# Kernel tuning notes

Hardware: AMD Instinct MI355X
Metric: run time of the kernel (lower is better)

## Reference

```python
import jax, jax.numpy as jnp
import numpy as np

B, T, V, E, H = 512, 40, 50000, 300, 512


def setup_inputs() -> dict:
    key = jax.random.key(0)
    ks = jax.random.split(key, 8)
    ref_expr_inds = jax.random.randint(ks[0], (B, T), 0, V)
    emb = jax.random.normal(ks[1], (V, E), dtype=jnp.float32) * 0.1
    w = lambda k, s: jax.random.normal(k, s, dtype=jnp.float32) * 0.05
    return dict(
        ref_expr_inds=ref_expr_inds,
        emb=emb,
        w_ih_f=w(ks[2], (3 * H, E)), w_hh_f=w(ks[3], (3 * H, H)),
        b_ih_f=jnp.zeros((3 * H,), jnp.float32), b_hh_f=jnp.zeros((3 * H,), jnp.float32),
        w_ih_b=w(ks[4], (3 * H, E)), w_hh_b=w(ks[5], (3 * H, H)),
        b_ih_b=jnp.zeros((3 * H,), jnp.float32), b_hh_b=jnp.zeros((3 * H,), jnp.float32),
    )


def _gru_dir(x, w_ih, w_hh, b_ih, b_hh):
    """Single-direction GRU (PyTorch math, gate order r,z,n). x: [B,T,E] -> [B,T,H]."""
    gi = jnp.einsum('bte,ge->btg', x, w_ih) + b_ih  # [B,T,3H], precomputed input gates

    def step(h, gi_t):
        gh = h @ w_hh.T + b_hh  # [B,3H]
        ir, iz, inn = jnp.split(gi_t, 3, axis=-1)
        hr, hz, hn = jnp.split(gh, 3, axis=-1)
        r = jax.nn.sigmoid(ir + hr)
        z = jax.nn.sigmoid(iz + hz)
        n = jnp.tanh(inn + r * hn)
        h_new = (1.0 - z) * n + z * h
        return h_new, h_new

    h0 = jnp.zeros((x.shape[0], w_hh.shape[1]), x.dtype)
    _, ys = jax.lax.scan(step, h0, jnp.swapaxes(gi, 0, 1))  # ys: [T,B,H]
    return jnp.swapaxes(ys, 0, 1)


def reference(ref_expr_inds, emb, w_ih_f, w_hh_f, b_ih_f, b_hh_f,
              w_ih_b, w_hh_b, b_ih_b, b_hh_b):
    valid = ref_expr_inds != 0  # True = real token (torch uses y_mask = (inds==0), then pools over ~y_mask)
    x = emb[ref_expr_inds]  # [B,T,E] embedding lookup
    y_f = _gru_dir(x, w_ih_f, w_hh_f, b_ih_f, b_hh_f)
    y_b = _gru_dir(x[:, ::-1], w_ih_b, w_hh_b, b_ih_b, b_hh_b)[:, ::-1]
    y_word = jnp.concatenate([y_f, y_b], axis=-1)  # [B,T,2H]
    neg = jnp.finfo(y_word.dtype).min
    # masked max-pool over valid tokens, vectorized (replaces python per-sample loop)
    y = jnp.max(jnp.where(valid[:, :, None], y_word, neg), axis=1, keepdims=True)  # [B,1,2H]
    return y
```

## Files before the change

kernel.cpp:

```cpp
#include <hip/hip_runtime.h>

typedef unsigned short u16;
typedef unsigned int u32;
typedef unsigned long long u64;
typedef short s16x8 __attribute__((ext_vector_type(8)));
typedef float f32x4 __attribute__((ext_vector_type(4)));
typedef u32 u32x4 __attribute__((ext_vector_type(4)));

#define T_SEQ 40
#define EMB 300
#define KPAD 320
#define NCOL 3072

__device__ __forceinline__ u16 f2bf(float x) {
  u32 u = __builtin_bit_cast(u32, x);
  u32 r = (u + 0x7fffu + ((u >> 16) & 1u)) >> 16;
  return (u16)r;
}
__device__ __forceinline__ float bf2f(u16 h) {
  return __builtin_bit_cast(float, ((u32)h) << 16);
}
#define LOG2E 1.4426950408889634f
__device__ __forceinline__ float sigm(float x) {
  return 1.0f / (1.0f + __builtin_amdgcn_exp2f(-x * LOG2E));
}
__device__ __forceinline__ float fast_tanh(float x) {
  return 1.0f - 2.0f / (1.0f + __builtin_amdgcn_exp2f(2.0f * LOG2E * x));
}

__global__ void k_init(const int* __restrict__ idxs, u64* __restrict__ mask,
                       int* __restrict__ bar) {
  int i = blockIdx.x * 256 + threadIdx.x;
  if (i < 264) __hip_atomic_store(&bar[i], 0, __ATOMIC_RELAXED, __HIP_MEMORY_SCOPE_AGENT);
  if (i < 512) {
    u64 b = 0;
    for (int t = 0; t < T_SEQ; ++t)
      if (idxs[i * T_SEQ + t] != 0) b |= (1ull << t);
    mask[i] = b;
  }
}

__global__ void k_prep_emb(const float* __restrict__ emb, u16* __restrict__ emb16) {
  for (int idx = blockIdx.x * 256 + threadIdx.x; idx < 50000 * 160; idx += 4096 * 256) {
    int row = idx / 160, c2 = idx - row * 160;
    int c0 = 2 * c2;
    float v0 = (c0 < EMB) ? emb[(size_t)row * EMB + c0] : 0.0f;
    float v1 = (c0 + 1 < EMB) ? emb[(size_t)row * EMB + c0 + 1] : 0.0f;
    ((u32*)emb16)[(size_t)row * 160 + c2] = (u32)f2bf(v0) | ((u32)f2bf(v1) << 16);
  }
}

__global__ void k_prep_wih(const float* __restrict__ wf, const float* __restrict__ wb,
                           u16* __restrict__ wih) {
  int n = blockIdx.x, e = threadIdx.x;
  int dir = (n >= 1536);
  int g = n - dir * 1536;
  const float* src = dir ? wb : wf;
  float v = (e < EMB) ? src[(size_t)g * EMB + e] : 0.0f;
  wih[(size_t)n * KPAD + e] = f2bf(v);
}

__global__ void k_prep_whh(const float* __restrict__ wf, const float* __restrict__ wb,
                           u16* __restrict__ w16) {
  int n = blockIdx.x, k = threadIdx.x;
  int dir = (n >= 1536);
  int g = n - dir * 1536;
  float v = (dir ? wb : wf)[(size_t)g * 512 + k];
  w16[(size_t)n * 512 + k] = f2bf(v);
}

__global__ void k_prep_bias(const float* __restrict__ bihf, const float* __restrict__ bihb,
                            const float* __restrict__ bhhf, const float* __restrict__ bhhb,
                            float* __restrict__ bias_ih, float* __restrict__ bias_hh) {
  int i = blockIdx.x * 1024 + threadIdx.x;
  if (i >= 3072) return;
  int dir = (i >= 1536);
  int g = i - dir * 1536;
  bias_ih[i] = dir ? bihb[g] : bihf[g];
  bias_hh[i] = dir ? bhhb[g] : bhhf[g];
}

__global__ __launch_bounds__(256) void k_gi_gemm(
    const int* __restrict__ idxs, const float* __restrict__ emb,
    const u16* __restrict__ emb16, int use_emb16,
    const u16* __restrict__ wih, const float* __restrict__ bias_ih,
    u16* __restrict__ gi) {
  __shared__ __align__(16) char smem[34816];
  u16(*As)[40] = (u16(*)[40])smem;
  u16(*Bs)[40] = (u16(*)[40])(smem + 10240);
  u16(*Cs)[136] = (u16(*)[136])smem;

  const int m0 = blockIdx.x * 128;
  const int n0 = blockIdx.y * 128;
  const int t = threadIdx.x;
  const int w = t >> 6, l = t & 63;
  const int wm = (w >> 1) * 64, wn = (w & 1) * 64;
  const int lr = l & 15, lg = l >> 4;

  f32x4 acc[4][4];
#pragma unroll
  for (int i = 0; i < 4; ++i)
#pragma unroll
    for (int j = 0; j < 4; ++j) acc[i][j] = (f32x4)0.0f;

  const int arow = t >> 1, aseg = t & 1;
  const int tok = idxs[m0 + arow];
  const float* aerow = emb + (size_t)tok * EMB;
  const u16* aerow16 = emb16 + (size_t)tok * KPAD;
  const u16* brow_p = wih + (size_t)(n0 + arow) * KPAD;

  for (int kc = 0; kc < 10; ++kc) {
    const int k0 = kc * 32;
    if (use_emb16) {
      *(uint4*)&As[arow][aseg * 16] = *(const uint4*)(aerow16 + k0 + aseg * 16);
      *(uint4*)(&As[arow][aseg * 16] + 8) = *(const uint4*)(aerow16 + k0 + aseg * 16 + 8);
    } else {
      int cb = k0 + aseg * 16;
      u16* d = &As[arow][aseg * 16];
      if (cb + 15 < EMB) {
        const float4* s = (const float4*)(aerow + cb);
        float4 v0 = s[0], v1 = s[1], v2 = s[2], v3 = s[3];
        uint4 w0, w1;
        w0.x = (u32)f2bf(v0.x) | ((u32)f2bf(v0.y) << 16);
        w0.y = (u32)f2bf(v0.z) | ((u32)f2bf(v0.w) << 16);
        w0.z = (u32)f2bf(v1.x) | ((u32)f2bf(v1.y) << 16);
        w0.w = (u32)f2bf(v1.z) | ((u32)f2bf(v1.w) << 16);
        w1.x = (u32)f2bf(v2.x) | ((u32)f2bf(v2.y) << 16);
        w1.y = (u32)f2bf(v2.z) | ((u32)f2bf(v2.w) << 16);
        w1.z = (u32)f2bf(v3.x) | ((u32)f2bf(v3.y) << 16);
        w1.w = (u32)f2bf(v3.z) | ((u32)f2bf(v3.w) << 16);
        *(uint4*)d = w0;
        *(uint4*)(d + 8) = w1;
      } else {
#pragma unroll
        for (int e = 0; e < 16; ++e) {
          int c = cb + e;
          d[e] = (c < EMB) ? f2bf(aerow[c]) : (u16)0;
        }
      }
    }
    {
      const u16* s = brow_p + k0 + aseg * 16;
      u16* d = &Bs[arow][aseg * 16];
      *(uint4*)d = *(const uint4*)s;
      *(uint4*)(d + 8) = *(const uint4*)(s + 8);
    }
    __syncthreads();
    s16x8 av[4], bv[4];
#pragma unroll
    for (int i = 0; i < 4; ++i) av[i] = *(const s16x8*)&As[wm + i * 16 + lr][lg * 8];
#pragma unroll
    for (int j = 0; j < 4; ++j) bv[j] = *(const s16x8*)&Bs[wn + j * 16 + lr][lg * 8];
#pragma unroll
    for (int i = 0; i < 4; ++i)
#pragma unroll
      for (int j = 0; j < 4; ++j)
        acc[i][j] = __builtin_amdgcn_mfma_f32_16x16x32_bf16(av[i], bv[j], acc[i][j], 0, 0, 0);
    __syncthreads();
  }

  float bj[4];
#pragma unroll
  for (int j = 0; j < 4; ++j) bj[j] = bias_ih[n0 + wn + j * 16 + lr];
#pragma unroll
  for (int i = 0; i < 4; ++i)
#pragma unroll
    for (int j = 0; j < 4; ++j)
#pragma unroll
      for (int r = 0; r < 4; ++r)
        Cs[wm + i * 16 + lg * 4 + r][wn + j * 16 + lr] = f2bf(acc[i][j][r] + bj[j]);
  __syncthreads();
#pragma unroll
  for (int rr = t >> 4; rr < 128; rr += 16) {
    const int cseg = (t & 15) * 8;
    __builtin_nontemporal_store(*(const u32x4*)&Cs[rr][cseg],
                                (u32x4*)(gi + (size_t)(m0 + rr) * NCOL + n0 + cseg));
  }
}

__global__ __launch_bounds__(512) void k_gru_persist(
    const u16* __restrict__ whh16, const float* __restrict__ bias_hh,
    const u16* __restrict__ gi, const u64* __restrict__ mask, u32* __restrict__ hpk,
    float* __restrict__ ymax, int* __restrict__ bar) {
  extern __shared__ u16 wlds[];
  __shared__ int s_claim[2];
  __shared__ int s_arrive;
  const int t = threadIdx.x;
  if (t == 0) {
    int xcd;
    asm volatile("s_getreg_b32 %0, hwreg(HW_REG_XCC_ID)" : "=s"(xcd));
    xcd &= 7;
    int slot =
        __hip_atomic_fetch_add(&bar[256 + xcd], 1, __ATOMIC_RELAXED, __HIP_MEMORY_SCOPE_AGENT);
    s_claim[0] = xcd;
    s_claim[1] = slot & 31;
    s_arrive = 0;
  }
  __syncthreads();
  const int mt = s_claim[0];
  const int slot = s_claim[1];
  const int dir = slot & 1;
  const int jt = slot >> 1;
  const int m0 = mt * 64, j0 = jt * 32;
  const int wbase = dir * 1536;
  const int w = t >> 6, l = t & 63, lr = l & 15, lg = l >> 4;
  const int mh = w >> 1, jh = w & 1;

  for (int c = t; c < 6144; c += 512) {
    const int col = c % 96, kcg = c / 96;
    const int g = col >> 5, jj = col & 31;
    const int k = (kcg >> 2) * 32 + (kcg & 3) * 8;
    const size_t off = (size_t)(wbase + g * 512 + j0 + jj) * 512 + k;
    *(uint4*)&wlds[c * 8] = *(const uint4*)(whh16 + off);
  }
  const int jg = j0 + jh * 16 + lr;
  const float bR = bias_hh[wbase + jg];
  const float bZ = bias_hh[wbase + 512 + jg];
  const float bN = bias_hh[wbase + 1024 + jg];
  u64 mk[4];
  float hprev[4], ym[4];
  int mrow[4];
#pragma unroll
  for (int r = 0; r < 4; ++r) {
    mrow[r] = m0 + mh * 16 + lg * 4 + r;
    mk[r] = mask[mrow[r]];
    hprev[r] = 0.0f;
    ym[r] = -3.402823466e38f;
  }
  __syncthreads();

  const int pollidx = mt * 32 + 2 * (l & 15) + dir;
  const size_t aoff = (size_t)(mh * 16 + lr) * 512;

  for (int s = 0; s < T_SEQ; ++s) {
    const int tok = dir ? (T_SEQ - 1 - s) : s;

    if (s > 0) {
      const u32 tgt = (u32)s;
      while (true) {
        u32 f = __hip_atomic_load((u32*)&bar[pollidx], __ATOMIC_RELAXED,
                                  __HIP_MEMORY_SCOPE_AGENT);
        if (__all(f >= tgt)) break;
        __builtin_amdgcn_s_sleep(1);
      }
    }

    u16 gr[4], gz[4], gn[4];
#pragma unroll
    for (int r = 0; r < 4; ++r) {
      const size_t gb = ((size_t)mrow[r] * T_SEQ + tok) * NCOL + wbase + jg;
      gr[r] = __builtin_nontemporal_load(gi + gb);
      gz[r] = __builtin_nontemporal_load(gi + gb + 512);
      gn[r] = __builtin_nontemporal_load(gi + gb + 1024);
    }

    f32x4 acc[3];
    acc[0] = acc[1] = acc[2] = (f32x4)0.0f;
    if (s > 0) {
      const u32* hs = hpk + ((((size_t)(s & 7)) * 2 + dir) * 8 + mt) * 32768;
#pragma unroll
      for (int kc = 0; kc < 16; ++kc) {
        const uint4* ap = (const uint4*)(hs + aoff + kc * 32 + lg * 8);
        uint4 q0 = ap[0], q1 = ap[1];
        u32 hw[8];
        *(uint4*)&hw[0] = q0;
        *(uint4*)&hw[4] = q1;
        u32 ahw[4], alw[4];
#pragma unroll
        for (int i = 0; i < 4; ++i) {
          ahw[i] = (hw[2 * i] & 0xFFFFu) | (hw[2 * i + 1] << 16);
          alw[i] = (hw[2 * i] >> 16) | (hw[2 * i + 1] & 0xFFFF0000u);
        }
        const s16x8 ah = __builtin_bit_cast(s16x8, *(uint4*)ahw);
        const s16x8 al = __builtin_bit_cast(s16x8, *(uint4*)alw);
        const int bb = ((kc * 4 + lg) * 96 + jh * 16 + lr) * 8;
#pragma unroll
        for (int g = 0; g < 3; ++g) {
          const s16x8 bh = *(const s16x8*)&wlds[bb + g * 256];
          acc[g] = __builtin_amdgcn_mfma_f32_16x16x32_bf16(ah, bh, acc[g], 0, 0, 0);
          acc[g] = __builtin_amdgcn_mfma_f32_16x16x32_bf16(al, bh, acc[g], 0, 0, 0);
        }
      }
    }

    u32 hpack[4];
#pragma unroll
    for (int r = 0; r < 4; ++r) {
      const float rg = sigm(bf2f(gr[r]) + acc[0][r] + bR);
      const float zg = sigm(bf2f(gz[r]) + acc[1][r] + bZ);
      const float ng = fast_tanh(bf2f(gn[r]) + rg * (acc[2][r] + bN));
      const float hn = (1.0f - zg) * ng + zg * hprev[r];
      hprev[r] = hn;
      const u16 hh = f2bf(hn);
      const u16 hl = f2bf(hn - bf2f(hh));
      hpack[r] = (u32)hh | ((u32)hl << 16);
      if ((mk[r] >> tok) & 1ull) ym[r] = fmaxf(ym[r], hn);
    }

    if (s < T_SEQ - 1) {
      u32* hd = hpk + ((((size_t)((s + 1) & 7)) * 2 + dir) * 8 + mt) * 32768;
#pragma unroll
      for (int r = 0; r < 4; ++r)
        hd[(size_t)(mh * 16 + lg * 4 + r) * 512 + jg] = hpack[r];
      asm volatile("s_waitcnt vmcnt(0)" ::: "memory");
      if (l == 0) {
        int old = atomicAdd(&s_arrive, 1);
        if (old == 8 * (s + 1) - 1)
          __hip_atomic_store((u32*)&bar[mt * 32 + slot], (u32)(s + 1), __ATOMIC_RELAXED,
                             __HIP_MEMORY_SCOPE_AGENT);
      }
    }
  }

#pragma unroll
  for (int r = 0; r < 4; ++r)
    ymax[(size_t)mrow[r] * 1024 + dir * 512 + jg] = ym[r];
}

extern "C" void kernel_launch(void* const* d_in, const int* in_sizes, int n_in,
                              void* d_out, int out_size, void* d_ws, size_t ws_size,
                              hipStream_t stream) {
  const int* idxs = (const int*)d_in[0];
  const float* emb = (const float*)d_in[1];
  const float* wihf = (const float*)d_in[2];
  const float* whhf = (const float*)d_in[3];
  const float* bihf = (const float*)d_in[4];
  const float* bhhf = (const float*)d_in[5];
  const float* wihb = (const float*)d_in[6];
  const float* whhb = (const float*)d_in[7];
  const float* bihb = (const float*)d_in[8];
  const float* bhhb = (const float*)d_in[9];
  float* ymax = (float*)d_out;

  char* ws = (char*)d_ws;
  u16* whh16 = (u16*)(ws + 0);
  u16* wih = (u16*)(ws + 6291456);
  float* bias_ih = (float*)(ws + 8257536);
  float* bias_hh = (float*)(ws + 8269824);
  u64* mask = (u64*)(ws + 8282112);
  int* bar = (int*)(ws + 8286208);
  u16* emb16 = (u16*)(ws + 8290304);
  u32* hpk = (u32*)(ws + 8290304);
  u16* gi = (u16*)(ws + 40290304);
  const int use_emb16 = (ws_size >= 166119424ull) ? 1 : 0;

  k_init<<<2, 256, 0, stream>>>(idxs, mask, bar);
  if (use_emb16) k_prep_emb<<<4096, 256, 0, stream>>>(emb, emb16);
  k_prep_wih<<<3072, 320, 0, stream>>>(wihf, wihb, wih);
  k_prep_whh<<<3072, 512, 0, stream>>>(whhf, whhb, whh16);
  k_prep_bias<<<3, 1024, 0, stream>>>(bihf, bihb, bhhf, bhhb, bias_ih, bias_hh);
  k_gi_gemm<<<dim3(160, 24), 256, 0, stream>>>(idxs, emb, emb16, use_emb16, wih, bias_ih, gi);

  hipFuncSetAttribute((const void*)k_gru_persist,
                      hipFuncAttributeMaxDynamicSharedMemorySize, 98304);
  k_gru_persist<<<dim3(256), dim3(512), 98304, stream>>>(whh16, bias_hh, gi, mask, hpk,
                                                         ymax, bar);
}
```

Before: 797.9 us.

## Remap persistent GRU work so each XCD owns one direction with 16-slot sync groups

Each XCD now handles one direction and a 128-row batch tile, and each block covers 32 hidden columns across all 8 waves. Previously an XCD held 64 rows for both directions in 32-block groups. Barrier groups shrink from 32 to 16 blocks, and blocks whose slot is 16 or above exit immediately. Other changes: the gate-input loads move ahead of the spin-wait so they overlap it, the s_sleep backoff becomes a busy FMA loop, and h-state loads are software-prefetched one k-chunk ahead. The aim is lower cross-block synchronization latency per timestep, at the cost of more MFMA work per wave and more idle launched blocks.

Measured after the change: 1.178 ms. 1.48x slower.

```diff
diff --git a/kernel.cpp b/kernel.cpp
--- a/kernel.cpp
+++ b/kernel.cpp
@@ -31,7 +31,7 @@
 __global__ void k_init(const int* __restrict__ idxs, u64* __restrict__ mask,
                        int* __restrict__ bar) {
   int i = blockIdx.x * 256 + threadIdx.x;
-  if (i < 264) __hip_atomic_store(&bar[i], 0, __ATOMIC_RELAXED, __HIP_MEMORY_SCOPE_AGENT);
+  if (i < 272) __hip_atomic_store(&bar[i], 0, __ATOMIC_RELAXED, __HIP_MEMORY_SCOPE_AGENT);
   if (i < 512) {
     u64 b = 0;
     for (int t = 0; t < T_SEQ; ++t)
@@ -193,18 +193,19 @@
     int slot =
         __hip_atomic_fetch_add(&bar[256 + xcd], 1, __ATOMIC_RELAXED, __HIP_MEMORY_SCOPE_AGENT);
     s_claim[0] = xcd;
-    s_claim[1] = slot & 31;
+    s_claim[1] = slot;
     s_arrive = 0;
   }
   __syncthreads();
-  const int mt = s_claim[0];
+  const int xcd = s_claim[0];
   const int slot = s_claim[1];
-  const int dir = slot & 1;
-  const int jt = slot >> 1;
-  const int m0 = mt * 64, j0 = jt * 32;
+  if (slot >= 16) return;
+
+  const int mt = xcd >> 1, dir = xcd & 1, jt = slot;
+  const int m0 = mt * 128, j0 = jt * 32;
   const int wbase = dir * 1536;
   const int w = t >> 6, l = t & 63, lr = l & 15, lg = l >> 4;
-  const int mh = w >> 1, jh = w & 1;
+  u32* flags = (u32*)bar + xcd * 16;
 
   for (int c = t; c < 6144; c += 512) {
     const int col = c % 96, kcg = c / 96;
@@ -213,58 +214,82 @@
     const size_t off = (size_t)(wbase + g * 512 + j0 + jj) * 512 + k;
     *(uint4*)&wlds[c * 8] = *(const uint4*)(whh16 + off);
   }
-  const int jg = j0 + jh * 16 + lr;
-  const float bR = bias_hh[wbase + jg];
-  const float bZ = bias_hh[wbase + 512 + jg];
-  const float bN = bias_hh[wbase + 1024 + jg];
+
+  int jg[2];
+  jg[0] = j0 + lr;
+  jg[1] = j0 + 16 + lr;
+  float bR[2], bZ[2], bN[2];
+#pragma unroll
+  for (int jn = 0; jn < 2; ++jn) {
+    bR[jn] = bias_hh[wbase + jg[jn]];
+    bZ[jn] = bias_hh[wbase + 512 + jg[jn]];
+    bN[jn] = bias_hh[wbase + 1024 + jg[jn]];
+  }
   u64 mk[4];
-  float hprev[4], ym[4];
   int mrow[4];
+  float hprev[2][4], ym[2][4];
 #pragma unroll
   for (int r = 0; r < 4; ++r) {
-    mrow[r] = m0 + mh * 16 + lg * 4 + r;
+    mrow[r] = m0 + w * 16 + lg * 4 + r;
     mk[r] = mask[mrow[r]];
-    hprev[r] = 0.0f;
-    ym[r] = -3.402823466e38f;
+#pragma unroll
+    for (int jn = 0; jn < 2; ++jn) {
+      hprev[jn][r] = 0.0f;
+      ym[jn][r] = -3.402823466e38f;
+    }
   }
   __syncthreads();
 
-  const int pollidx = mt * 32 + 2 * (l & 15) + dir;
-  const size_t aoff = (size_t)(mh * 16 + lr) * 512;
+  const size_t arow = (size_t)(w * 16 + lr) * 512 + lg * 8;
+  const u32* fp = &flags[l & 15];
 
   for (int s = 0; s < T_SEQ; ++s) {
     const int tok = dir ? (T_SEQ - 1 - s) : s;
 
+    u16 gr[2][4], gz[2][4], gn[2][4];
+#pragma unroll
+    for (int jn = 0; jn < 2; ++jn)
+#pragma unroll
+      for (int r = 0; r < 4; ++r) {
+        const size_t gb = ((size_t)mrow[r] * T_SEQ + tok) * NCOL + wbase + jg[jn];
+        gr[jn][r] = __builtin_nontemporal_load(gi + gb);
+        gz[jn][r] = __builtin_nontemporal_load(gi + gb + 512);
+        gn[jn][r] = __builtin_nontemporal_load(gi + gb + 1024);
+      }
+
+    f32x4 acc[3][2];
+#pragma unroll
+    for (int g = 0; g < 3; ++g) acc[g][0] = acc[g][1] = (f32x4)0.0f;
+
     if (s > 0) {
-      const u32 tgt = (u32)s;
-      while (true) {
-        u32 f = __hip_atomic_load((u32*)&bar[pollidx], __ATOMIC_RELAXED,
-                                  __HIP_MEMORY_SCOPE_AGENT);
-        if (__all(f >= tgt)) break;
-        __builtin_amdgcn_s_sleep(1);
-      }
-    }
-
-    u16 gr[4], gz[4], gn[4];
-#pragma unroll
-    for (int r = 0; r < 4; ++r) {
-      const size_t gb = ((size_t)mrow[r] * T_SEQ + tok) * NCOL + wbase + jg;
-      gr[r] = __builtin_nontemporal_load(gi + gb);
-      gz[r] = __builtin_nontemporal_load(gi + gb + 512);
-      gn[r] = __builtin_nontemporal_load(gi + gb + 1024);
-    }
-
-    f32x4 acc[3];
-    acc[0] = acc[1] = acc[2] = (f32x4)0.0f;
-    if (s > 0) {
-      const u32* hs = hpk + ((((size_t)(s & 7)) * 2 + dir) * 8 + mt) * 32768;
+      {
+        const u32 tgt = (u32)s;
+        float ba = 1.0000001f;
+        const float bm = 1.0000002f;
+        while (true) {
+          u32 f = __hip_atomic_load(fp, __ATOMIC_RELAXED, __HIP_MEMORY_SCOPE_AGENT);
+          if (__all(f >= tgt)) break;
+#pragma unroll
+          for (int b = 0; b < 24; ++b)
+            asm volatile("v_fmac_f32 %0, %1, %1" : "+v"(ba) : "v"(bm));
+        }
+        asm volatile("" ::"v"(ba));
+      }
+
+      const u32* hs = hpk + ((size_t)((s & 7) * 2 + dir) * 4 + mt) * 65536;
+      const u32* ap = hs + arow;
+      uint4 c0 = *(const uint4*)(ap);
+      uint4 c1 = *(const uint4*)(ap + 4);
 #pragma unroll
       for (int kc = 0; kc < 16; ++kc) {
-        const uint4* ap = (const uint4*)(hs + aoff + kc * 32 + lg * 8);
-        uint4 q0 = ap[0], q1 = ap[1];
+        uint4 n0 = c0, n1 = c1;
+        if (kc < 15) {
+          n0 = *(const uint4*)(ap + (kc + 1) * 32);
+          n1 = *(const uint4*)(ap + (kc + 1) * 32 + 4);
+        }
         u32 hw[8];
-        *(uint4*)&hw[0] = q0;
-        *(uint4*)&hw[4] = q1;
+        *(uint4*)&hw[0] = c0;
+        *(uint4*)&hw[4] = c1;
         u32 ahw[4], alw[4];
 #pragma unroll
         for (int i = 0; i < 4; ++i) {
@@ -273,48 +298,65 @@
         }
         const s16x8 ah = __builtin_bit_cast(s16x8, *(uint4*)ahw);
         const s16x8 al = __builtin_bit_cast(s16x8, *(uint4*)alw);
-        const int bb = ((kc * 4 + lg) * 96 + jh * 16 + lr) * 8;
-#pragma unroll
-        for (int g = 0; g < 3; ++g) {
-          const s16x8 bh = *(const s16x8*)&wlds[bb + g * 256];
-          acc[g] = __builtin_amdgcn_mfma_f32_16x16x32_bf16(ah, bh, acc[g], 0, 0, 0);
-          acc[g] = __builtin_amdgcn_mfma_f32_16x16x32_bf16(al, bh, acc[g], 0, 0, 0);
+        const int bb = (kc * 4 + lg) * 96;
+#pragma unroll
+        for (int g = 0; g < 3; ++g)
+#pragma unroll
+          for (int jn = 0; jn < 2; ++jn) {
+            const s16x8 bh = *(const s16x8*)&wlds[(bb + g * 32 + jn * 16 + lr) * 8];
+            acc[g][jn] = __builtin_amdgcn_mfma_f32_16x16x32_bf16(ah, bh, acc[g][jn], 0, 0, 0);
+            acc[g][jn] = __builtin_amdgcn_mfma_f32_16x16x32_bf16(al, bh, acc[g][jn], 0, 0, 0);
+          }
+        c0 = n0;
+        c1 = n1;
+      }
+    }
+
+    float hn_v[2][4];
+#pragma unroll
+    for (int jn = 0; jn < 2; ++jn)
+#pragma unroll
+      for (int r = 0; r < 4; ++r) {
+        const float rg = sigm(bf2f(gr[jn][r]) + acc[0][jn][r] + bR[jn]);
+        const float zg = sigm(bf2f(gz[jn][r]) + acc[1][jn][r] + bZ[jn]);
+        const float ng = fast_tanh(bf2f(gn[jn][r]) + rg * (acc[2][jn][r] + bN[jn]));
+        hn_v[jn][r] = (1.0f - zg) * ng + zg * hprev[jn][r];
+      }
+
+    if (s < T_SEQ - 1) {
+      u32* hd = hpk + ((size_t)(((s + 1) & 7) * 2 + dir) * 4 + mt) * 65536;
+#pragma unroll
+      for (int jn = 0; jn < 2; ++jn)
+#pragma unroll
+        for (int r = 0; r < 4; ++r) {
+          const float hn = hn_v[jn][r];
+          const u16 hh = f2bf(hn);
+          const u16 hl = f2bf(hn - bf2f(hh));
+          hd[(size_t)(w * 16 + lg * 4 + r) * 512 + jg[jn]] = (u32)hh | ((u32)hl << 16);
         }
-      }
-    }
-
-    u32 hpack[4];
-#pragma unroll
-    for (int r = 0; r < 4; ++r) {
-      const float rg = sigm(bf2f(gr[r]) + acc[0][r] + bR);
-      const float zg = sigm(bf2f(gz[r]) + acc[1][r] + bZ);
-      const float ng = fast_tanh(bf2f(gn[r]) + rg * (acc[2][r] + bN));
-      const float hn = (1.0f - zg) * ng + zg * hprev[r];
-      hprev[r] = hn;
-      const u16 hh = f2bf(hn);
-      const u16 hl = f2bf(hn - bf2f(hh));
-      hpack[r] = (u32)hh | ((u32)hl << 16);
-      if ((mk[r] >> tok) & 1ull) ym[r] = fmaxf(ym[r], hn);
-    }
-
-    if (s < T_SEQ - 1) {
-      u32* hd = hpk + ((((size_t)((s + 1) & 7)) * 2 + dir) * 8 + mt) * 32768;
-#pragma unroll
-      for (int r = 0; r < 4; ++r)
-        hd[(size_t)(mh * 16 + lg * 4 + r) * 512 + jg] = hpack[r];
       asm volatile("s_waitcnt vmcnt(0)" ::: "memory");
       if (l == 0) {
         int old = atomicAdd(&s_arrive, 1);
         if (old == 8 * (s + 1) - 1)
-          __hip_atomic_store((u32*)&bar[mt * 32 + slot], (u32)(s + 1), __ATOMIC_RELAXED,
+          __hip_atomic_store(&flags[slot], (u32)(s + 1), __ATOMIC_RELAXED,
                              __HIP_MEMORY_SCOPE_AGENT);
       }
     }
-  }
-
-#pragma unroll
-  for (int r = 0; r < 4; ++r)
-    ymax[(size_t)mrow[r] * 1024 + dir * 512 + jg] = ym[r];
+
+#pragma unroll
+    for (int jn = 0; jn < 2; ++jn)
+#pragma unroll
+      for (int r = 0; r < 4; ++r) {
+        if ((mk[r] >> tok) & 1ull) ym[jn][r] = fmaxf(ym[jn][r], hn_v[jn][r]);
+        hprev[jn][r] = hn_v[jn][r];
+      }
+  }
+
+#pragma unroll
+  for (int jn = 0; jn < 2; ++jn)
+#pragma unroll
+    for (int r = 0; r < 4; ++r)
+      ymax[(size_t)mrow[r] * 1024 + dir * 512 + jg[jn]] = ym[jn][r];
 }
 
 extern "C" void kernel_launch(void* const* d_in, const int* in_sizes, int n_in,
```

## Replace persistent GRU kernel with per-timestep launches instead of global spin barriers

Applied to the files above, without the earlier changes.

Removes the persistent kernel with its XCD-based slot claiming and atomic flag polling between blocks. The recurrence now runs as 40 separate step launches, each reloading its W_hh tile into LDS and ping-ponging h through two global buffers. The running max is kept in the output buffer instead of registers. This drops the spin-wait synchronisation in exchange for launch overhead, a W_hh reload every step, and extra global read-modify-write traffic on the output.

Result: slower. 862.6 us (+8.1%).

```diff
diff --git a/kernel.cpp b/kernel.cpp
--- a/kernel.cpp
+++ b/kernel.cpp
@@ -26,18 +26,6 @@
 }
 __device__ __forceinline__ float fast_tanh(float x) {
   return 1.0f - 2.0f / (1.0f + __builtin_amdgcn_exp2f(2.0f * LOG2E * x));
-}
-
-__global__ void k_init(const int* __restrict__ idxs, u64* __restrict__ mask,
-                       int* __restrict__ bar) {
-  int i = blockIdx.x * 256 + threadIdx.x;
-  if (i < 264) __hip_atomic_store(&bar[i], 0, __ATOMIC_RELAXED, __HIP_MEMORY_SCOPE_AGENT);
-  if (i < 512) {
-    u64 b = 0;
-    for (int t = 0; t < T_SEQ; ++t)
-      if (idxs[i * T_SEQ + t] != 0) b |= (1ull << t);
-    mask[i] = b;
-  }
 }
 
 __global__ void k_prep_emb(const float* __restrict__ emb, u16* __restrict__ emb16) {
@@ -178,143 +166,109 @@
   }
 }
 
-__global__ __launch_bounds__(512) void k_gru_persist(
+__global__ __launch_bounds__(512) void k_step(
     const u16* __restrict__ whh16, const float* __restrict__ bias_hh,
-    const u16* __restrict__ gi, const u64* __restrict__ mask, u32* __restrict__ hpk,
-    float* __restrict__ ymax, int* __restrict__ bar) {
-  extern __shared__ u16 wlds[];
-  __shared__ int s_claim[2];
-  __shared__ int s_arrive;
-  const int t = threadIdx.x;
-  if (t == 0) {
-    int xcd;
-    asm volatile("s_getreg_b32 %0, hwreg(HW_REG_XCC_ID)" : "=s"(xcd));
-    xcd &= 7;
-    int slot =
-        __hip_atomic_fetch_add(&bar[256 + xcd], 1, __ATOMIC_RELAXED, __HIP_MEMORY_SCOPE_AGENT);
-    s_claim[0] = xcd;
-    s_claim[1] = slot & 31;
-    s_arrive = 0;
-  }
-  __syncthreads();
-  const int mt = s_claim[0];
-  const int slot = s_claim[1];
-  const int dir = slot & 1;
-  const int jt = slot >> 1;
-  const int m0 = mt * 64, j0 = jt * 32;
+    const u16* __restrict__ gi, const int* __restrict__ idxs,
+    u32* __restrict__ hpk, float* __restrict__ ymax, int s) {
+  extern __shared__ u16 blds[];
+  const int m0 = blockIdx.x * 64, j0 = blockIdx.y * 32;
+  const int dir = blockIdx.z;
   const int wbase = dir * 1536;
-  const int w = t >> 6, l = t & 63, lr = l & 15, lg = l >> 4;
-  const int mh = w >> 1, jh = w & 1;
-
-  for (int c = t; c < 6144; c += 512) {
-    const int col = c % 96, kcg = c / 96;
-    const int g = col >> 5, jj = col & 31;
-    const int k = (kcg >> 2) * 32 + (kcg & 3) * 8;
-    const size_t off = (size_t)(wbase + g * 512 + j0 + jj) * 512 + k;
-    *(uint4*)&wlds[c * 8] = *(const uint4*)(whh16 + off);
-  }
+  const int t = threadIdx.x, w = t >> 6, l = t & 63, lr = l & 15, lg = l >> 4;
+  const int mq = w >> 1, jh = w & 1;
+  const int tok = dir ? (T_SEQ - 1 - s) : s;
+
+  const u32* hs = hpk + (size_t)((s & 1) * 2 + dir) * 262144;
+  u32* hd = hpk + (size_t)(((s + 1) & 1) * 2 + dir) * 262144;
+
+  if (s > 0) {
+    for (int c = t; c < 6144; c += 512) {
+      const int rr = c >> 6, kseg = c & 63;
+      const int g = rr >> 5, jj = rr & 31;
+      *(uint4*)&blds[((size_t)kseg * 96 + g * 32 + jj) * 8] =
+          *(const uint4*)(whh16 + (size_t)(wbase + g * 512 + j0 + jj) * 512 + kseg * 8);
+    }
+  }
+
   const int jg = j0 + jh * 16 + lr;
+  int mrow[4], msk[4];
+  u16 gr[4], gz[4], gn[4];
+  float hp[4];
+#pragma unroll
+  for (int r = 0; r < 4; ++r) {
+    mrow[r] = m0 + mq * 16 + lg * 4 + r;
+    const size_t gb = ((size_t)mrow[r] * T_SEQ + tok) * NCOL + wbase + jg;
+    gr[r] = __builtin_nontemporal_load(gi + gb);
+    gz[r] = __builtin_nontemporal_load(gi + gb + 512);
+    gn[r] = __builtin_nontemporal_load(gi + gb + 1024);
+    msk[r] = idxs[mrow[r] * T_SEQ + tok];
+    if (s > 0) {
+      const u32 v = hs[(size_t)mrow[r] * 512 + jg];
+      hp[r] = bf2f((u16)(v & 0xFFFFu)) + bf2f((u16)(v >> 16));
+    } else {
+      hp[r] = 0.0f;
+    }
+  }
   const float bR = bias_hh[wbase + jg];
   const float bZ = bias_hh[wbase + 512 + jg];
   const float bN = bias_hh[wbase + 1024 + jg];
-  u64 mk[4];
-  float hprev[4], ym[4];
-  int mrow[4];
+
+  f32x4 acc[3];
+  acc[0] = acc[1] = acc[2] = (f32x4)0.0f;
+
+  if (s > 0) {
+    __syncthreads();
+    const u32* ap = hs + (size_t)(m0 + mq * 16 + lr) * 512 + lg * 8;
+    uint4 c0 = *(const uint4*)ap;
+    uint4 c1 = *(const uint4*)(ap + 4);
+#pragma unroll
+    for (int kc = 0; kc < 16; ++kc) {
+      uint4 n0 = c0, n1 = c1;
+      if (kc < 15) {
+        n0 = *(const uint4*)(ap + (kc + 1) * 32);
+        n1 = *(const uint4*)(ap + (kc + 1) * 32 + 4);
+      }
+      u32 hw[8];
+      *(uint4*)&hw[0] = c0;
+      *(uint4*)&hw[4] = c1;
+      u32 ahw[4], alw[4];
+#pragma unroll
+      for (int i = 0; i < 4; ++i) {
+        ahw[i] = (hw[2 * i] & 0xFFFFu) | (hw[2 * i + 1] << 16);
+        alw[i] = (hw[2 * i] >> 16) | (hw[2 * i + 1] & 0xFFFF0000u);
+      }
+      const s16x8 ah = __builtin_bit_cast(s16x8, *(uint4*)ahw);
+      const s16x8 al = __builtin_bit_cast(s16x8, *(uint4*)alw);
+      const int bb = ((kc * 4 + lg) * 96 + jh * 16 + lr) * 8;
+#pragma unroll
+      for (int g = 0; g < 3; ++g) {
+        const s16x8 bh = *(const s16x8*)&blds[bb + g * 256];
+        acc[g] = __builtin_amdgcn_mfma_f32_16x16x32_bf16(ah, bh, acc[g], 0, 0, 0);
+        acc[g] = __builtin_amdgcn_mfma_f32_16x16x32_bf16(al, bh, acc[g], 0, 0, 0);
+      }
+      c0 = n0;
+      c1 = n1;
+    }
+  }
+
 #pragma unroll
   for (int r = 0; r < 4; ++r) {
-    mrow[r] = m0 + mh * 16 + lg * 4 + r;
-    mk[r] = mask[mrow[r]];
-    hprev[r] = 0.0f;
-    ym[r] = -3.402823466e38f;
-  }
-  __syncthreads();
-
-  const int pollidx = mt * 32 + 2 * (l & 15) + dir;
-  const size_t aoff = (size_t)(mh * 16 + lr) * 512;
-
-  for (int s = 0; s < T_SEQ; ++s) {
-    const int tok = dir ? (T_SEQ - 1 - s) : s;
-
-    if (s > 0) {
-      const u32 tgt = (u32)s;
-      while (true) {
-        u32 f = __hip_atomic_load((u32*)&bar[pollidx], __ATOMIC_RELAXED,
-                                  __HIP_MEMORY_SCOPE_AGENT);
-        if (__all(f >= tgt)) break;
-        __builtin_amdgcn_s_sleep(1);
-      }
-    }
-
-    u16 gr[4], gz[4], gn[4];
-#pragma unroll
-    for (int r = 0; r < 4; ++r) {
-      const size_t gb = ((size_t)mrow[r] * T_SEQ + tok) * NCOL + wbase + jg;
-      gr[r] = __builtin_nontemporal_load(gi + gb);
-      gz[r] = __builtin_nontemporal_load(gi + gb + 512);
-      gn[r] = __builtin_nontemporal_load(gi + gb + 1024);
-    }
-
-    f32x4 acc[3];
-    acc[0] = acc[1] = acc[2] = (f32x4)0.0f;
-    if (s > 0) {
-      const u32* hs = hpk + ((((size_t)(s & 7)) * 2 + dir) * 8 + mt) * 32768;
-#pragma unroll
-      for (int kc = 0; kc < 16; ++kc) {
-        const uint4* ap = (const uint4*)(hs + aoff + kc * 32 + lg * 8);
-        uint4 q0 = ap[0], q1 = ap[1];
-        u32 hw[8];
-        *(uint4*)&hw[0] = q0;
-        *(uint4*)&hw[4] = q1;
-        u32 ahw[4], alw[4];
-#pragma unroll
-        for (int i = 0; i < 4; ++i) {
-          ahw[i] = (hw[2 * i] & 0xFFFFu) | (hw[2 * i + 1] << 16);
-          alw[i] = (hw[2 * i] >> 16) | (hw[2 * i + 1] & 0xFFFF0000u);
-        }
-        const s16x8 ah = __builtin_bit_cast(s16x8, *(uint4*)ahw);
-        const s16x8 al = __builtin_bit_cast(s16x8, *(uint4*)alw);
-        const int bb = ((kc * 4 + lg) * 96 + jh * 16 + lr) * 8;
-#pragma unroll
-        for (int g = 0; g < 3; ++g) {
-          const s16x8 bh = *(const s16x8*)&wlds[bb + g * 256];
-          acc[g] = __builtin_amdgcn_mfma_f32_16x16x32_bf16(ah, bh, acc[g], 0, 0, 0);
-          acc[g] = __builtin_amdgcn_mfma_f32_16x16x32_bf16(al, bh, acc[g], 0, 0, 0);
-        }
-      }
-    }
-
-    u32 hpack[4];
-#pragma unroll
-    for (int r = 0; r < 4; ++r) {
-      const float rg = sigm(bf2f(gr[r]) + acc[0][r] + bR);
-      const float zg = sigm(bf2f(gz[r]) + acc[1][r] + bZ);
-      const float ng = fast_tanh(bf2f(gn[r]) + rg * (acc[2][r] + bN));
-      const float hn = (1.0f - zg) * ng + zg * hprev[r];
-      hprev[r] = hn;
+    const float rg = sigm(bf2f(gr[r]) + acc[0][r] + bR);
+    const float zg = sigm(bf2f(gz[r]) + acc[1][r] + bZ);
+    const float ng = fast_tanh(bf2f(gn[r]) + rg * (acc[2][r] + bN));
+    const float hn = (1.0f - zg) * ng + zg * hp[r];
+    if (s < T_SEQ - 1) {
       const u16 hh = f2bf(hn);
       const u16 hl = f2bf(hn - bf2f(hh));
-      hpack[r] = (u32)hh | ((u32)hl << 16);
-      if ((mk[r] >> tok) & 1ull) ym[r] = fmaxf(ym[r], hn);
-    }
-
-    if (s < T_SEQ - 1) {
-      u32* hd = hpk + ((((size_t)((s + 1) & 7)) * 2 + dir) * 8 + mt) * 32768;
-#pragma unroll
-      for (int r = 0; r < 4; ++r)
-        hd[(size_t)(mh * 16 + lg * 4 + r) * 512 + jg] = hpack[r];
-      asm volatile("s_waitcnt vmcnt(0)" ::: "memory");
-      if (l == 0) {
-        int old = atomicAdd(&s_arrive, 1);
-        if (old == 8 * (s + 1) - 1)
-          __hip_atomic_store((u32*)&bar[mt * 32 + slot], (u32)(s + 1), __ATOMIC_RELAXED,
-                             __HIP_MEMORY_SCOPE_AGENT);
-      }
-    }
-  }
-
-#pragma unroll
-  for (int r = 0; r < 4; ++r)
-    ymax[(size_t)mrow[r] * 1024 + dir * 512 + jg] = ym[r];
+      hd[(size_t)mrow[r] * 512 + jg] = (u32)hh | ((u32)hl << 16);
+    }
+    float* yp = ymax + (size_t)mrow[r] * 1024 + dir * 512 + jg;
+    if (s == 0) {
+      *yp = msk[r] ? hn : -3.402823466e38f;
+    } else if (msk[r]) {
+      *yp = fmaxf(*yp, hn);
+    }
+  }
 }
 
 extern "C" void kernel_launch(void* const* d_in, const int* in_sizes, int n_in,
@@ -337,22 +291,19 @@
   u16* wih = (u16*)(ws + 6291456);
   float* bias_ih = (float*)(ws + 8257536);
   float* bias_hh = (float*)(ws + 8269824);
-  u64* mask = (u64*)(ws + 8282112);
-  int* bar = (int*)(ws + 8286208);
   u16* emb16 = (u16*)(ws + 8290304);
   u32* hpk = (u32*)(ws + 8290304);
   u16* gi = (u16*)(ws + 40290304);
   const int use_emb16 = (ws_size >= 166119424ull) ? 1 : 0;
 
-  k_init<<<2, 256, 0, stream>>>(idxs, mask, bar);
   if (use_emb16) k_prep_emb<<<4096, 256, 0, stream>>>(emb, emb16);
   k_prep_wih<<<3072, 320, 0, stream>>>(wihf, wihb, wih);
   k_prep_whh<<<3072, 512, 0, stream>>>(whhf, whhb, whh16);
   k_prep_bias<<<3, 1024, 0, stream>>>(bihf, bihb, bhhf, bhhb, bias_ih, bias_hh);
   k_gi_gemm<<<dim3(160, 24), 256, 0, stream>>>(idxs, emb, emb16, use_emb16, wih, bias_ih, gi);
 
-  hipFuncSetAttribute((const void*)k_gru_persist,
-                      hipFuncAttributeMaxDynamicSharedMemorySize, 98304);
-  k_gru_persist<<<dim3(256), dim3(512), 98304, stream>>>(whh16, bias_hh, gi, mask, hpk,
-                                                         ymax, bar);
-}
+  hipFuncSetAttribute((const void*)k_step, hipFuncAttributeMaxDynamicSharedMemorySize,
+                      98304);
+  for (int s = 0; s < T_SEQ; ++s)
+    k_step<<<dim3(8, 16, 2), 512, 98304, stream>>>(whh16, bias_hh, gi, idxs, hpk, ymax, s);
+}
```
